# Optimization experiments

Hardware: AMD Instinct MI355X
Metric: run time of the kernel (lower is better)

Reference implementation:

```python
import jax, jax.numpy as jnp
import numpy as np

# Dimensions
B, C, H, W = 16, 256, 32, 32
CO, DK, DV, NH = 256, 128, 128, 8   # channels_out, depth_k, depth_v, num_heads
KS = 3                              # conv kernel size
DKH, DVH = DK // NH, DV // NH


def setup_inputs() -> dict:
    key = jax.random.key(0)
    ks = jax.random.split(key, 4)
    s = 0.05
    return {
        "x": jax.random.normal(ks[0], (B, C, H, W), jnp.float32),
        # conv branch: 3x3 conv -> channels_out - depth_v = 128, HWIO layout
        "conv_w": jax.random.normal(ks[1], (KS, KS, C, CO - DV), jnp.float32) * s,
        "conv_b": jnp.zeros((CO - DV,), jnp.float32),
        # 1x1 QKV conv: 2*depth_k + depth_v output channels
        "qkv_w": jax.random.normal(ks[2], (2 * DK + DV, C), jnp.float32) * s,
        "qkv_b": jnp.zeros((2 * DK + DV,), jnp.float32),
        # 1x1 output projection conv: depth_v -> depth_v
        "proj_w": jax.random.normal(ks[3], (DV, DV), jnp.float32) * s,
        "proj_b": jnp.zeros((DV,), jnp.float32),
    }


def reference(x, conv_w, conv_b, qkv_w, qkv_b, proj_w, proj_b):
    # --- conv branch (3x3, SAME padding, NCHW) ---
    conv_out = jax.lax.conv_general_dilated(
        x, conv_w, window_strides=(1, 1), padding='SAME',
        dimension_numbers=('NCHW', 'HWIO', 'NCHW'))
    conv_out = conv_out + conv_b[None, :, None, None]

    # --- attention branch ---
    # 1x1 conv == channel matmul
    kqv = jnp.einsum('bchw,oc->bohw', x, qkv_w) + qkv_b[None, :, None, None]
    # tf.split order: k, q, v
    k, q, v = jnp.split(kqv, [DK, 2 * DK], axis=1)
    q = q * (DKH ** -0.5)

    def heads(t, d):  # (B, NH*d, H, W) -> (B, NH, H*W, d)
        return t.reshape(B, NH, d, H * W).transpose(0, 1, 3, 2)

    qh, kh, vh = heads(q, DKH), heads(k, DKH), heads(v, DVH)
    logits = jnp.einsum('bnqd,bnkd->bnqk', qh, kh)          # (B,NH,HW,HW)
    weights = jax.nn.softmax(logits, axis=-1)
    attn = jnp.einsum('bnqk,bnkd->bnqd', weights, vh)       # (B,NH,HW,DVH)
    # combine heads, head-major channel order -> (B, DV, H, W)
    attn = attn.transpose(0, 1, 3, 2).reshape(B, DV, H, W)
    attn_out = jnp.einsum('bchw,oc->bohw', attn, proj_w) + proj_b[None, :, None, None]

    return jnp.concatenate([conv_out, attn_out], axis=1)
```

## Files before the change

kernel.cpp:

```cpp
#include <hip/hip_runtime.h>
#include <hip/hip_bf16.h>


#define Bn   16
#define Cin  256
#define HWp  1024
#define COn  256
#define NHn  8

typedef short short8  __attribute__((ext_vector_type(8)));
typedef short short4v __attribute__((ext_vector_type(4)));
typedef float f32x4   __attribute__((ext_vector_type(4)));
typedef float f32x16  __attribute__((ext_vector_type(16)));

__device__ inline short bf16_rne(float f) {
  unsigned u = __builtin_bit_cast(unsigned, f);
  u += 0x7fffu + ((u >> 16) & 1u);
  return (short)(u >> 16);
}

__device__ inline unsigned pkbf(float a, float b) {
  __hip_bfloat162 h = __float22bfloat162_rn(make_float2(a, b));
  unsigned u;
  __builtin_memcpy(&u, &h, 4);
  return u;
}

__device__ inline void store_bf8(short* dst, const float* f) {
  uint4 u;
  u.x = pkbf(f[0], f[1]); u.y = pkbf(f[2], f[3]);
  u.z = pkbf(f[4], f[5]); u.w = pkbf(f[6], f[7]);
  *(uint4*)dst = u;
}

__global__ __launch_bounds__(256) void prep_all(
    const float* __restrict__ cw, const float* __restrict__ qw,
    const float* __restrict__ pw, short* __restrict__ wfc,
    short* __restrict__ wfq, short* __restrict__ wfp)
{
  const int gid  = blockIdx.x * 256 + threadIdx.x;
  const int lane = gid & 63, frag = gid >> 6;
  const int l15 = lane & 15, q = lane >> 4;
  short8 pk;
  if (frag < 576) {
    const int cf = frag & 7, cq = (frag >> 3) & 7, kk = frag >> 6;
    const int co = cf * 16 + l15, c = cq * 32 + q * 8;
#pragma unroll
    for (int j = 0; j < 8; ++j)
      pk[j] = bf16_rne(cw[(size_t)(kk * Cin + c + j) * 128 + co]);
    *(short8*)(wfc + (size_t)frag * 512 + lane * 8) = pk;
  } else if (frag < 768) {
    const int f = frag - 576;
    const int rt = f >> 3, kf = f & 7;
    const int o = rt * 16 + l15, c = kf * 32 + q * 8;
#pragma unroll
    for (int j = 0; j < 8; ++j) pk[j] = bf16_rne(qw[o * Cin + c + j]);
    *(short8*)(wfq + (size_t)f * 512 + lane * 8) = pk;
  } else if (frag < 800) {
    const int f = frag - 768;
    const int rt = f >> 2, kf = f & 3;
    const int o = rt * 16 + l15, c = kf * 32 + q * 8;
#pragma unroll
    for (int j = 0; j < 8; ++j) pk[j] = bf16_rne(pw[o * 128 + c + j]);
    *(short8*)(wfp + (size_t)f * 512 + lane * 8) = pk;
  }
}

__global__ __launch_bounds__(512) void conv_mfma(
    const float* __restrict__ x, const short* __restrict__ wf,
    const float* __restrict__ bias, float* __restrict__ out)
{
  __shared__ short xl[5440];
  const int tid  = threadIdx.x;
  const int lane = tid & 63, wv = tid >> 6;
  const int l15  = lane & 15, g = lane >> 4;
  const int mtile = blockIdx.x;
  const int b  = mtile >> 4;
  const int h0 = (mtile & 15) * 2;

  f32x4 acc[4] = {};

  for (int c0 = 0; c0 < Cin; c0 += 32) {
    __syncthreads();
    for (int ch = tid; ch < 544; ch += 512) {
      const int cell = ch >> 2, qq = ch & 3;
      const int r = cell / 34, col = cell - r * 34;
      const int h_in = h0 - 1 + r, w_in = col - 1;
      const bool v = (h_in >= 0) & (h_in < 32) & (w_in >= 0) & (w_in < 32);
      const float* xp = x + (size_t)(b * Cin + c0 + qq * 8) * HWp
                          + h_in * 32 + w_in;
      float fv[8];
#pragma unroll
      for (int j = 0; j < 8; ++j) fv[j] = v ? xp[j * HWp] : 0.f;
      store_bf8(&xl[cell * 40 + qq * 8], fv);
    }
    __syncthreads();

    const int cq = c0 >> 5;
#pragma unroll
    for (int kk = 0; kk < 9; ++kk) {
      const int kh = kk / 3, kw = kk - kh * 3;
      const short8 a0 = *(const short8*)(wf + (size_t)((kk * 8 + cq) * 8 + wv) * 512 + lane * 8);
#pragma unroll
      for (int bf = 0; bf < 4; ++bf) {
        const int m = bf * 16 + l15;
        const int r = (m >> 5) + kh, col = (m & 31) + kw;
        const short8 xv = *(const short8*)&xl[(r * 34 + col) * 40 + g * 8];
        acc[bf] = __builtin_amdgcn_mfma_f32_16x16x32_bf16(a0, xv, acc[bf], 0, 0, 0);
      }
    }
  }

  const int cob = wv * 16 + g * 4;
#pragma unroll
  for (int r = 0; r < 4; ++r) {
    const int co = cob + r;
    const float bv = bias[co];
    float* op = out + (size_t)(b * COn + co) * HWp + h0 * 32 + l15;
#pragma unroll
    for (int bf = 0; bf < 4; ++bf)
      op[bf * 16] = acc[bf][r] + bv;
  }
}

__global__ __launch_bounds__(512) void qkv_mfma(
    const float* __restrict__ x, const short* __restrict__ wfq,
    const float* __restrict__ bias, short* __restrict__ qbuf,
    short* __restrict__ kbuf, short* __restrict__ vtbuf)
{
  __shared__ short xl[16384];
  const int tid = threadIdx.x, lane = tid & 63, wv = tid >> 6;
  const int l15 = lane & 15, g = lane >> 4;
  const int hw0 = blockIdx.x * 64;
  const int b   = blockIdx.y;

#pragma unroll
  for (int it = 0; it < 4; ++it) {
    const int p  = it * 512 + tid;
    const int mt = p >> 9, kf = (p >> 6) & 7, qq = (p >> 4) & 3, hl = p & 15;
    const float* xp = x + (size_t)(b * Cin + kf * 32 + qq * 8) * HWp
                        + hw0 + mt * 16 + hl;
    float fv[8];
#pragma unroll
    for (int j = 0; j < 8; ++j) fv[j] = xp[(size_t)j * HWp];
    store_bf8(&xl[p * 8], fv);
  }
  __syncthreads();

  f32x4 acc[3][4] = {};
  for (int kf = 0; kf < 8; ++kf) {
    short8 bfr[4];
#pragma unroll
    for (int mt = 0; mt < 4; ++mt)
      bfr[mt] = *(const short8*)&xl[(((mt * 8 + kf) * 4 + g) * 16 + l15) * 8];
#pragma unroll
    for (int i = 0; i < 3; ++i) {
      const int rt = wv * 3 + i;
      const short8 af = *(const short8*)(wfq + ((size_t)(rt * 8 + kf) * 64 + lane) * 8);
#pragma unroll
      for (int mt = 0; mt < 4; ++mt)
        acc[i][mt] = __builtin_amdgcn_mfma_f32_16x16x32_bf16(af, bfr[mt], acc[i][mt], 0, 0, 0);
    }
  }

#pragma unroll
  for (int i = 0; i < 3; ++i) {
    const int rt = wv * 3 + i;
    float bv[4];
#pragma unroll
    for (int r = 0; r < 4; ++r) bv[r] = bias[rt * 16 + 4 * g + r];
    if (rt < 8) {
      short* kp = kbuf + ((size_t)(b * NHn + rt) * HWp + hw0) * 16 + 4 * g;
#pragma unroll
      for (int mt = 0; mt < 4; ++mt) {
        short4v s;
#pragma unroll
        for (int r = 0; r < 4; ++r) s[r] = bf16_rne(acc[i][mt][r] + bv[r]);
        *(short4v*)(kp + (size_t)(mt * 16 + l15) * 16) = s;
      }
    } else if (rt < 16) {
      short* qp = qbuf + ((size_t)(b * NHn + rt - 8) * HWp + hw0) * 16 + 4 * g;
#pragma unroll
      for (int mt = 0; mt < 4; ++mt) {
        short4v s;
#pragma unroll
        for (int r = 0; r < 4; ++r) s[r] = bf16_rne((acc[i][mt][r] + bv[r]) * 0.25f);
        *(short4v*)(qp + (size_t)(mt * 16 + l15) * 16) = s;
      }
    } else {
      short* vp = vtbuf + (size_t)(b * NHn + rt - 16) * 16 * HWp;
#pragma unroll
      for (int mt = 0; mt < 4; ++mt)
#pragma unroll
        for (int r = 0; r < 4; ++r)
          vp[(size_t)(4 * g + r) * HWp + hw0 + mt * 16 + l15] =
              bf16_rne(acc[i][mt][r] + bv[r]);
    }
  }
}

__global__ __launch_bounds__(256) void attn_mfma(
    const short* __restrict__ qb, const short* __restrict__ kb,
    const short* __restrict__ vt, float* __restrict__ abuf)
{
  __shared__ short P[4][2][32][40];
  const int tid = threadIdx.x, lane = tid & 63, wv = tid >> 6;
  const int l15 = lane & 15, g = lane >> 4;
  const int l31 = lane & 31, hi = lane >> 5;
  const int h = blockIdx.y, b = blockIdx.z, bh = b * NHn + h;
  const int q0 = blockIdx.x * 128 + wv * 32;

  const short* qp = qb + (size_t)bh * HWp * 16;
  const short* kp = kb + (size_t)bh * HWp * 16;
  const short* vp = vt + (size_t)bh * 16 * HWp;

  const short8 qf = *(const short8*)(qp + (size_t)(q0 + l31) * 16 + hi * 8);

  f32x4 o0 = {}, o1 = {};
  float lsum = 0.f;

  for (int kt = 0; kt < HWp; kt += 64) {
#pragma unroll
    for (int t = 0; t < 2; ++t) {
      const int k0 = kt + t * 32;
      const short8 kf = *(const short8*)(kp + (size_t)(k0 + l31) * 16 + hi * 8);
      f32x16 z = {};
      const f32x16 s = __builtin_amdgcn_mfma_f32_32x32x16_bf16(kf, qf, z, 0, 0, 0);
      float p[16];
#pragma unroll
      for (int r = 0; r < 16; ++r) { p[r] = __expf(s[r]); lsum += p[r]; }
#pragma unroll
      for (int rg = 0; rg < 4; ++rg) {
        uint2 u;
        u.x = pkbf(p[4 * rg + 0], p[4 * rg + 1]);
        u.y = pkbf(p[4 * rg + 2], p[4 * rg + 3]);
        *(uint2*)&P[wv][t][l31][8 * rg + 4 * hi] = u;
      }
      const short8 vf = *(const short8*)(vp + (size_t)l15 * HWp + k0 + g * 8);
      const short8 pf0 = *(const short8*)&P[wv][t][l15][g * 8];
      o0 = __builtin_amdgcn_mfma_f32_16x16x32_bf16(vf, pf0, o0, 0, 0, 0);
      const short8 pf1 = *(const short8*)&P[wv][t][16 + l15][g * 8];
      o1 = __builtin_amdgcn_mfma_f32_16x16x32_bf16(vf, pf1, o1, 0, 0, 0);
    }
  }

  const float l  = lsum + __shfl_xor(lsum, 32);
  const float li0 = 1.f / __shfl(l, l15);
  const float li1 = 1.f / __shfl(l, 16 + l15);
#pragma unroll
  for (int r = 0; r < 4; ++r) {
    const int d = 4 * g + r;
    float* op = abuf + (size_t)(b * 128 + h * 16 + d) * HWp + q0;
    op[l15]      = o0[r] * li0;
    op[16 + l15] = o1[r] * li1;
  }
}

__global__ __launch_bounds__(256) void proj_mfma(
    const float* __restrict__ a, const short* __restrict__ wfp,
    const float* __restrict__ bias, float* __restrict__ out)
{
  __shared__ short xl[8192];
  const int tid = threadIdx.x, lane = tid & 63, wv = tid >> 6;
  const int l15 = lane & 15, g = lane >> 4;
  const int hw0 = blockIdx.x * 64;
  const int b   = blockIdx.y;

#pragma unroll
  for (int it = 0; it < 4; ++it) {
    const int p  = it * 256 + tid;
    const int mt = p >> 8, kf = (p >> 6) & 3, qq = (p >> 4) & 3, hl = p & 15;
    const float* ap = a + (size_t)(b * 128 + kf * 32 + qq * 8) * HWp
                        + hw0 + mt * 16 + hl;
    float fv[8];
#pragma unroll
    for (int j = 0; j < 8; ++j) fv[j] = ap[(size_t)j * HWp];
    store_bf8(&xl[p * 8], fv);
  }
  __syncthreads();

  f32x4 acc[2][4] = {};
  for (int kf = 0; kf < 4; ++kf) {
    short8 bfr[4];
#pragma unroll
    for (int mt = 0; mt < 4; ++mt)
      bfr[mt] = *(const short8*)&xl[(((mt * 4 + kf) * 4 + g) * 16 + l15) * 8];
#pragma unroll
    for (int i = 0; i < 2; ++i) {
      const int rt = wv * 2 + i;
      const short8 af = *(const short8*)(wfp + ((size_t)(rt * 4 + kf) * 64 + lane) * 8);
#pragma unroll
      for (int mt = 0; mt < 4; ++mt)
        acc[i][mt] = __builtin_amdgcn_mfma_f32_16x16x32_bf16(af, bfr[mt], acc[i][mt], 0, 0, 0);
    }
  }

#pragma unroll
  for (int i = 0; i < 2; ++i) {
    const int rt = wv * 2 + i;
#pragma unroll
    for (int r = 0; r < 4; ++r) {
      const int o = rt * 16 + 4 * g + r;
      const float bv = bias[o];
      float* op = out + (size_t)(b * COn + 128 + o) * HWp + hw0 + l15;
#pragma unroll
      for (int mt = 0; mt < 4; ++mt)
        op[mt * 16] = acc[i][mt][r] + bv;
    }
  }
}

extern "C" void kernel_launch(void* const* d_in, const int* in_sizes, int n_in,
                              void* d_out, int out_size, void* d_ws, size_t ws_size,
                              hipStream_t stream) {
  const float* x      = (const float*)d_in[0];
  const float* conv_w = (const float*)d_in[1];
  const float* conv_b = (const float*)d_in[2];
  const float* qkv_w  = (const float*)d_in[3];
  const float* qkv_b  = (const float*)d_in[4];
  const float* proj_w = (const float*)d_in[5];
  const float* proj_b = (const float*)d_in[6];
  float* out = (float*)d_out;

  char* wsb = (char*)d_ws;
  short* wfc    = (short*)wsb;
  short* wfq    = (short*)(wsb + (1u << 20));
  short* wfp    = (short*)(wsb + (2u << 20));
  short* qbuf16 = (short*)(wsb + (8u << 20));
  short* kbuf16 = (short*)(wsb + (12u << 20));
  short* vtbuf  = (short*)(wsb + (16u << 20));
  float* abuf   = (float*)(wsb + (20u << 20));

  prep_all  <<<dim3(200), 256, 0, stream>>>(conv_w, qkv_w, proj_w, wfc, wfq, wfp);
  conv_mfma <<<dim3(256), 512, 0, stream>>>(x, wfc, conv_b, out);
  qkv_mfma  <<<dim3(16, 16), 512, 0, stream>>>(x, wfq, qkv_b, qbuf16, kbuf16, vtbuf);
  attn_mfma <<<dim3(8, 8, 16), 256, 0, stream>>>(qbuf16, kbuf16, vtbuf, abuf);
  proj_mfma <<<dim3(16, 16), 256, 0, stream>>>(abuf, wfp, proj_b, out);
}
```

Baseline: 165.9 us.

## Pre-transpose x to channel-last bf16 and double-buffer conv staging

Adds a prep_x kernel that converts x once into a bf16 channel-last buffer. The conv and QKV kernels then load 16-byte vectors from that buffer instead of doing strided fp32 gathers with a conversion in each kernel. The conv kernel double-buffers its shared-memory tiles so the next chunk's load overlaps the current MFMAs, and pads the tile rows; the QKV kernel adds an XOR swizzle to its shared-memory layout to reduce bank conflicts. The cost is an extra kernel launch and an extra pass writing and reading the transposed copy of x.

```diff
diff --git a/kernel.cpp b/kernel.cpp
--- a/kernel.cpp
+++ b/kernel.cpp
@@ -66,37 +66,64 @@
   }
 }
 
+__global__ __launch_bounds__(256) void prep_x(
+    const float* __restrict__ x, short* __restrict__ xt)
+{
+  __shared__ short t[32][262];
+  const int tid = threadIdx.x;
+  const int hw0 = (blockIdx.x & 3) * 256;
+  const int c0  = ((blockIdx.x >> 2) & 7) * 32;
+  const int b   = blockIdx.x >> 5;
+
+#pragma unroll 4
+  for (int cc = 0; cc < 32; ++cc)
+    t[cc][tid] = bf16_rne(x[(size_t)(b * Cin + c0 + cc) * HWp + hw0 + tid]);
+  __syncthreads();
+
+  for (int s = tid; s < 1024; s += 256) {
+    const int hwl = s >> 2, q4 = s & 3;
+    short8 pk;
+#pragma unroll
+    for (int j = 0; j < 8; ++j) pk[j] = t[q4 * 8 + j][hwl];
+    *(short8*)&xt[((size_t)(b * HWp + hw0 + hwl)) * 256 + c0 + q4 * 8] = pk;
+  }
+}
+
 __global__ __launch_bounds__(512) void conv_mfma(
-    const float* __restrict__ x, const short* __restrict__ wf,
+    const short* __restrict__ xt, const short* __restrict__ wf,
     const float* __restrict__ bias, float* __restrict__ out)
 {
-  __shared__ short xl[5440];
+  __shared__ short xl[2][5712];
   const int tid  = threadIdx.x;
   const int lane = tid & 63, wv = tid >> 6;
   const int l15  = lane & 15, g = lane >> 4;
-  const int mtile = blockIdx.x;
-  const int b  = mtile >> 4;
-  const int h0 = (mtile & 15) * 2;
+  const int b  = blockIdx.x >> 4;
+  const int h0 = (blockIdx.x & 15) * 2;
 
   f32x4 acc[4] = {};
 
-  for (int c0 = 0; c0 < Cin; c0 += 32) {
-    __syncthreads();
-    for (int ch = tid; ch < 544; ch += 512) {
-      const int cell = ch >> 2, qq = ch & 3;
-      const int r = cell / 34, col = cell - r * 34;
-      const int h_in = h0 - 1 + r, w_in = col - 1;
-      const bool v = (h_in >= 0) & (h_in < 32) & (w_in >= 0) & (w_in < 32);
-      const float* xp = x + (size_t)(b * Cin + c0 + qq * 8) * HWp
-                          + h_in * 32 + w_in;
-      float fv[8];
-#pragma unroll
-      for (int j = 0; j < 8; ++j) fv[j] = v ? xp[j * HWp] : 0.f;
-      store_bf8(&xl[cell * 40 + qq * 8], fv);
-    }
-    __syncthreads();
-
-    const int cq = c0 >> 5;
+#define STAGE(chunk)                                                          \
+  {                                                                           \
+    const int c0_ = (chunk) * 32;                                             \
+    short* dst_ = xl[(chunk) & 1];                                            \
+    for (int s = tid; s < 544; s += 512) {                                    \
+      const int cell = s >> 2, qq = s & 3;                                    \
+      const int r = cell / 34, col = cell - r * 34;                           \
+      const int h_in = h0 - 1 + r, w_in = col - 1;                            \
+      short8 v = {};                                                          \
+      if (h_in >= 0 && h_in < 32 && w_in >= 0 && w_in < 32)                   \
+        v = *(const short8*)&xt[((size_t)(b * HWp + h_in * 32 + w_in)) * 256  \
+                                + c0_ + qq * 8];                              \
+      *(short8*)&dst_[cell * 42 + qq * 8] = v;                                \
+    }                                                                         \
+  }
+
+  STAGE(0);
+  __syncthreads();
+
+  for (int cq = 0; cq < 8; ++cq) {
+    if (cq < 7) STAGE(cq + 1);
+    const short* cur = xl[cq & 1];
 #pragma unroll
     for (int kk = 0; kk < 9; ++kk) {
       const int kh = kk / 3, kw = kk - kh * 3;
@@ -105,11 +132,13 @@
       for (int bf = 0; bf < 4; ++bf) {
         const int m = bf * 16 + l15;
         const int r = (m >> 5) + kh, col = (m & 31) + kw;
-        const short8 xv = *(const short8*)&xl[(r * 34 + col) * 40 + g * 8];
+        const short8 xv = *(const short8*)&cur[(r * 34 + col) * 42 + g * 8];
         acc[bf] = __builtin_amdgcn_mfma_f32_16x16x32_bf16(a0, xv, acc[bf], 0, 0, 0);
       }
     }
-  }
+    __syncthreads();
+  }
+#undef STAGE
 
   const int cob = wv * 16 + g * 4;
 #pragma unroll
@@ -124,7 +153,7 @@
 }
 
 __global__ __launch_bounds__(512) void qkv_mfma(
-    const float* __restrict__ x, const short* __restrict__ wfq,
+    const short* __restrict__ xt, const short* __restrict__ wfq,
     const float* __restrict__ bias, short* __restrict__ qbuf,
     short* __restrict__ kbuf, short* __restrict__ vtbuf)
 {
@@ -134,16 +163,16 @@
   const int hw0 = blockIdx.x * 64;
   const int b   = blockIdx.y;
 
-#pragma unroll
-  for (int it = 0; it < 4; ++it) {
-    const int p  = it * 512 + tid;
-    const int mt = p >> 9, kf = (p >> 6) & 7, qq = (p >> 4) & 3, hl = p & 15;
-    const float* xp = x + (size_t)(b * Cin + kf * 32 + qq * 8) * HWp
-                        + hw0 + mt * 16 + hl;
-    float fv[8];
-#pragma unroll
-    for (int j = 0; j < 8; ++j) fv[j] = xp[(size_t)j * HWp];
-    store_bf8(&xl[p * 8], fv);
+  {
+    const int qq = tid & 3, kf = (tid >> 2) & 7, hl = tid >> 5;
+#pragma unroll
+    for (int mt = 0; mt < 4; ++mt) {
+      const int p  = ((mt * 8 + kf) * 4 + qq) * 16 + hl;
+      const int sw = p ^ ((p >> 4) & 7);
+      const short8 v = *(const short8*)&xt[((size_t)(b * HWp + hw0 + mt * 16 + hl)) * 256
+                                           + kf * 32 + qq * 8];
+      *(short8*)&xl[sw * 8] = v;
+    }
   }
   __syncthreads();
 
@@ -151,8 +180,11 @@
   for (int kf = 0; kf < 8; ++kf) {
     short8 bfr[4];
 #pragma unroll
-    for (int mt = 0; mt < 4; ++mt)
-      bfr[mt] = *(const short8*)&xl[(((mt * 8 + kf) * 4 + g) * 16 + l15) * 8];
+    for (int mt = 0; mt < 4; ++mt) {
+      const int q  = ((mt * 8 + kf) * 4 + g) * 16 + l15;
+      const int sw = q ^ ((q >> 4) & 7);
+      bfr[mt] = *(const short8*)&xl[sw * 8];
+    }
 #pragma unroll
     for (int i = 0; i < 3; ++i) {
       const int rt = wv * 3 + i;
@@ -330,10 +362,12 @@
   short* kbuf16 = (short*)(wsb + (12u << 20));
   short* vtbuf  = (short*)(wsb + (16u << 20));
   float* abuf   = (float*)(wsb + (20u << 20));
+  short* xtbuf  = (short*)(wsb + (28u << 20));
 
   prep_all  <<<dim3(200), 256, 0, stream>>>(conv_w, qkv_w, proj_w, wfc, wfq, wfp);
-  conv_mfma <<<dim3(256), 512, 0, stream>>>(x, wfc, conv_b, out);
-  qkv_mfma  <<<dim3(16, 16), 512, 0, stream>>>(x, wfq, qkv_b, qbuf16, kbuf16, vtbuf);
+  prep_x    <<<dim3(512), 256, 0, stream>>>(x, xtbuf);
+  conv_mfma <<<dim3(256), 512, 0, stream>>>(xtbuf, wfc, conv_b, out);
+  qkv_mfma  <<<dim3(16, 16), 512, 0, stream>>>(xtbuf, wfq, qkv_b, qbuf16, kbuf16, vtbuf);
   attn_mfma <<<dim3(8, 8, 16), 256, 0, stream>>>(qbuf16, kbuf16, vtbuf, abuf);
   proj_mfma <<<dim3(16, 16), 256, 0, stream>>>(abuf, wfp, proj_b, out);
 }
```

Measured after the change: 182.5 us. 1.1x slower.
